# Kernel tuning notes

Measured on AMD Instinct MI355X. Metric: run time of the kernel, lower is better.

The kernel has to match this reference:

```python
import jax, jax.numpy as jnp
import numpy as np


def setup_inputs() -> dict:
    key = jax.random.key(0)
    # values near 1 so a 4096-long cumulative product stays numerically sane
    x = 1.0 + 0.001 * jax.random.normal(key, (32, 4096, 512), dtype=jnp.float32)
    return {"x": x, "dim": 1}


def reference(x, dim):
    # cumulative product along `dim` (inclusive scan), same math as torch.cumprod
    return jnp.cumprod(x, axis=dim)
```

## Files before the change

kernel.cpp:

```cpp
#include <hip/hip_runtime.h>


constexpr int L  = 4096;
constexpr int C  = 512;
constexpr int C4 = C / 4;
constexpr int CG = 8;
constexpr int W  = 64;
constexpr int KE = 8;
constexpr int CL = W * KE;
constexpr int NCHUNK = L / CL;

__device__ __forceinline__ float4 mul4(float4 a, float4 b) {
    return make_float4(a.x * b.x, a.y * b.y, a.z * b.z, a.w * b.w);
}

__global__ __launch_bounds__(CG * W, 4)
void cumprod_kernel(const float4* __restrict__ x, float4* __restrict__ out) {
    __shared__ float4 s[W][CG + 1];

    const int tid = threadIdx.x;
    const int c4  = tid & (CG - 1);
    const int w   = tid >> 3;
    const int c4g = blockIdx.x * CG + c4;
    const int b   = blockIdx.y;

    const int base = (b * L) * C4 + c4g;

    float4 carry = make_float4(1.f, 1.f, 1.f, 1.f);

    for (int chunk = 0; chunk < NCHUNK; ++chunk) {
        const int lbase = base + (chunk * CL + w * KE) * C4;

        float4 v[KE];
#pragma unroll
        for (int i = 0; i < KE; ++i) v[i] = x[lbase + i * C4];

#pragma unroll
        for (int i = 1; i < KE; ++i) v[i] = mul4(v[i], v[i - 1]);

        s[w][c4] = v[KE - 1];
        __syncthreads();
#pragma unroll
        for (int d = 1; d < W; d <<= 1) {
            float4 t;
            bool act = (w >= d);
            if (act) t = s[w - d][c4];
            __syncthreads();
            if (act) s[w][c4] = mul4(s[w][c4], t);
            __syncthreads();
        }

        float4 excl = carry;
        if (w > 0) excl = mul4(excl, s[w - 1][c4]);
        const float4 total = s[W - 1][c4];

#pragma unroll
        for (int i = 0; i < KE; ++i) {
            out[lbase + i * C4] = mul4(excl, v[i]);
        }

        carry = mul4(carry, total);
        __syncthreads();
    }
}

extern "C" void kernel_launch(void* const* d_in, const int* in_sizes, int n_in,
                              void* d_out, int out_size, void* d_ws, size_t ws_size,
                              hipStream_t stream) {
    const float4* x = (const float4*)d_in[0];
    float4* out = (float4*)d_out;

    const int B = in_sizes[0] / (L * C);

    dim3 grid(C4 / CG, B);
    dim3 block(CG * W);
    cumprod_kernel<<<grid, block, 0, stream>>>(x, out);
}
```

Baseline: 463.9 us.

## Replace shared-memory block scan with wave shuffles and prefetch next chunk

Swaps the 64-step shared-memory Hillis-Steele scan, which needed two barriers per step, for an intra-wave shuffle scan plus a small per-wave totals exchange through double-buffered shared memory, leaving one barrier per chunk. It also register-double-buffers the input loads so the next chunk's reads are issued before the current chunk is computed. Together these aim to cut barrier overhead and hide load latency in a memory-bound scan. The cost is higher register pressure from two buffers of eight float4 values each, and full unrolling of the chunk loop, which could reduce occupancy.

```diff
diff --git a/kernel.cpp b/kernel.cpp
--- a/kernel.cpp
+++ b/kernel.cpp
@@ -5,62 +5,92 @@
 constexpr int C  = 512;
 constexpr int C4 = C / 4;
 constexpr int CG = 8;
-constexpr int W  = 64;
 constexpr int KE = 8;
-constexpr int CL = W * KE;
+constexpr int NW = 8;
+constexpr int SW = 8;
+constexpr int WTH = NW * SW;
+constexpr int CL  = WTH * KE;
 constexpr int NCHUNK = L / CL;
 
 __device__ __forceinline__ float4 mul4(float4 a, float4 b) {
     return make_float4(a.x * b.x, a.y * b.y, a.z * b.z, a.w * b.w);
 }
 
-__global__ __launch_bounds__(CG * W, 4)
+__device__ __forceinline__ float4 shfl_up4(float4 v, int d) {
+    float4 r;
+    r.x = __shfl_up(v.x, d, 64);
+    r.y = __shfl_up(v.y, d, 64);
+    r.z = __shfl_up(v.z, d, 64);
+    r.w = __shfl_up(v.w, d, 64);
+    return r;
+}
+
+__global__ __launch_bounds__(512, 4)
 void cumprod_kernel(const float4* __restrict__ x, float4* __restrict__ out) {
-    __shared__ float4 s[W][CG + 1];
+    __shared__ float4 swt[2][NW][CG];
 
-    const int tid = threadIdx.x;
-    const int c4  = tid & (CG - 1);
-    const int w   = tid >> 3;
-    const int c4g = blockIdx.x * CG + c4;
-    const int b   = blockIdx.y;
-
-    const int base = (b * L) * C4 + c4g;
+    const int tid  = threadIdx.x;
+    const int c4   = tid & (CG - 1);
+    const int w    = tid >> 3;
+    const int wave = tid >> 6;
+    const int wl   = (tid >> 3) & (SW - 1);
+    const int c4g  = blockIdx.x * CG + c4;
+    const int b    = blockIdx.y;
+    const int base = b * L * C4 + c4g;
 
     float4 carry = make_float4(1.f, 1.f, 1.f, 1.f);
+    float4 buf[2][KE];
 
+    {
+        const int lb = base + (w * KE) * C4;
+#pragma unroll
+        for (int i = 0; i < KE; ++i) buf[0][i] = x[lb + i * C4];
+    }
+
+#pragma unroll
     for (int chunk = 0; chunk < NCHUNK; ++chunk) {
-        const int lbase = base + (chunk * CL + w * KE) * C4;
+        const int cur = chunk & 1;
+        const int nxt = cur ^ 1;
 
-        float4 v[KE];
+        if (chunk + 1 < NCHUNK) {
+            const int lb = base + ((chunk + 1) * CL + w * KE) * C4;
 #pragma unroll
-        for (int i = 0; i < KE; ++i) v[i] = x[lbase + i * C4];
+            for (int i = 0; i < KE; ++i) buf[nxt][i] = x[lb + i * C4];
+        }
+
+        float4* v = buf[cur];
 
 #pragma unroll
         for (int i = 1; i < KE; ++i) v[i] = mul4(v[i], v[i - 1]);
 
-        s[w][c4] = v[KE - 1];
+        float4 p = v[KE - 1];
+#pragma unroll
+        for (int d = 1; d < SW; d <<= 1) {
+            float4 t = shfl_up4(p, d * CG);
+            if (wl >= d) p = mul4(p, t);
+        }
+        float4 ew = shfl_up4(p, CG);
+        if (wl == 0) ew = make_float4(1.f, 1.f, 1.f, 1.f);
+
+        if (wl == SW - 1) swt[cur][wave][c4] = p;
         __syncthreads();
+
+        float4 wpref = make_float4(1.f, 1.f, 1.f, 1.f);
+        float4 btot  = make_float4(1.f, 1.f, 1.f, 1.f);
 #pragma unroll
-        for (int d = 1; d < W; d <<= 1) {
-            float4 t;
-            bool act = (w >= d);
-            if (act) t = s[w - d][c4];
-            __syncthreads();
-            if (act) s[w][c4] = mul4(s[w][c4], t);
-            __syncthreads();
+        for (int j = 0; j < NW; ++j) {
+            float4 t = swt[cur][j][c4];
+            if (j < wave) wpref = mul4(wpref, t);
+            btot = mul4(btot, t);
         }
 
-        float4 excl = carry;
-        if (w > 0) excl = mul4(excl, s[w - 1][c4]);
-        const float4 total = s[W - 1][c4];
+        const float4 excl = mul4(mul4(carry, wpref), ew);
 
+        const int lb = base + (chunk * CL + w * KE) * C4;
 #pragma unroll
-        for (int i = 0; i < KE; ++i) {
-            out[lbase + i * C4] = mul4(excl, v[i]);
-        }
+        for (int i = 0; i < KE; ++i) out[lb + i * C4] = mul4(excl, v[i]);
 
-        carry = mul4(carry, total);
-        __syncthreads();
+        carry = mul4(carry, btot);
     }
 }
 
@@ -73,6 +103,6 @@
     const int B = in_sizes[0] / (L * C);
 
     dim3 grid(C4 / CG, B);
-    dim3 block(CG * W);
+    dim3 block(512);
     cumprod_kernel<<<grid, block, 0, stream>>>(x, out);
 }
```

Result: slower. 546.7 us (+17.9%).
